# Kernel tuning notes

Hardware: AMD Instinct MI355X
Metric: run time of the kernel (lower is better)

The kernel has to match this reference:

```python
import jax, jax.numpy as jnp
import numpy as np

V, H, O = 50257, 1024, 1024
B, T = 64, 256

def setup_inputs() -> dict:
    key = jax.random.key(0)
    ks = jax.random.split(key, 8)
    s = 1.0 / np.sqrt(H)
    return {
        "input": jax.random.randint(ks[0], (B, T), 0, V),
        "hidden": jnp.zeros((B, H), jnp.float32),
        "emb": jax.random.normal(ks[1], (V, H), jnp.float32),
        "Wi": jax.random.uniform(ks[2], (H, H), jnp.float32, -s, s),
        "bi": jax.random.uniform(ks[3], (H,), jnp.float32, -s, s),
        "Wh": jax.random.uniform(ks[4], (H, H), jnp.float32, -s, s),
        "bh": jax.random.uniform(ks[5], (H,), jnp.float32, -s, s),
        "Wo": jax.random.uniform(ks[6], (H, O), jnp.float32, -s, s),
        "bo": jax.random.uniform(ks[7], (O,), jnp.float32, -s, s),
    }

def reference(input, hidden, emb, Wi, bi, Wh, bh, Wo, bo):
    # embedded: [B, T, H]; precompute the input-to-hidden projection for all steps
    embedded = emb[input]
    ix = jnp.einsum('bth,hk->tbk', embedded, Wi) + bi  # [T, B, H]

    def step(h, ix_t):
        h = jnp.tanh(ix_t + h @ Wh + bh)
        out = h @ Wo + bo
        return h, out

    hidden, outs = jax.lax.scan(step, hidden, ix)  # outs: [T, B, O]
    output_seq = jnp.transpose(outs, (1, 0, 2))    # [B, T, O]
    return output_seq, hidden
```

## Files before the change

### kernel.cpp

```cpp
#include <hip/hip_runtime.h>

typedef unsigned short u16;
typedef unsigned long long u64;
typedef short v8s __attribute__((ext_vector_type(8)));
typedef float v4f __attribute__((ext_vector_type(4)));

__device__ __forceinline__ u16 f2bf(float x) {
    union { float f; unsigned u; } v; v.f = x;
    unsigned r = v.u + 0x7fffu + ((v.u >> 16) & 1u);
    return (u16)(r >> 16);
}

__global__ __launch_bounds__(256) void convert_w(
    const float* __restrict__ Wi, const float* __restrict__ Wh,
    const float* __restrict__ Wo, u16* __restrict__ wi_t,
    u16* __restrict__ wh_t, u16* __restrict__ wo_t) {
    const float* src; u16* dst;
    if (blockIdx.y == 0)      { src = Wi; dst = wi_t; }
    else if (blockIdx.y == 1) { src = Wh; dst = wh_t; }
    else                      { src = Wo; dst = wo_t; }
    int k0 = (blockIdx.x & 31) * 32;
    int n0 = (blockIdx.x >> 5) * 32;
    __shared__ float tile[32][33];
    int t = threadIdx.x;
    {
        int kl = t >> 3, nl4 = (t & 7) * 4;
        float4 v = *(const float4*)(src + (size_t)(k0 + kl) * 1024 + n0 + nl4);
        tile[kl][nl4 + 0] = v.x; tile[kl][nl4 + 1] = v.y;
        tile[kl][nl4 + 2] = v.z; tile[kl][nl4 + 3] = v.w;
    }
    __syncthreads();
    {
        int nl = t >> 3, kl4 = (t & 7) * 4;
        ushort4 o;
        o.x = f2bf(tile[kl4 + 0][nl]); o.y = f2bf(tile[kl4 + 1][nl]);
        o.z = f2bf(tile[kl4 + 2][nl]); o.w = f2bf(tile[kl4 + 3][nl]);
        *(ushort4*)(dst + (size_t)(n0 + nl) * 1024 + k0 + kl4) = o;
    }
}

__global__ __launch_bounds__(256) void gather_emb(
    const int* __restrict__ input, const float* __restrict__ emb,
    u16* __restrict__ Aemb) {
    int r = blockIdx.x * 4 + (threadIdx.x >> 6);
    int lane = threadIdx.x & 63;
    int b = r & 63, t = r >> 6;
    int idx = input[b * 256 + t];
    const float* s = emb + (size_t)idx * 1024;
    u16* d = Aemb + (size_t)r * 1024;
#pragma unroll
    for (int i = 0; i < 4; i++) {
        float4 v = *(const float4*)(s + i * 256 + lane * 4);
        ushort4 o;
        o.x = f2bf(v.x); o.y = f2bf(v.y); o.z = f2bf(v.z); o.w = f2bf(v.w);
        *(ushort4*)(d + i * 256 + lane * 4) = o;
    }
}

__global__ __launch_bounds__(256) void gemm_bias(
    const u16* __restrict__ A, const u16* __restrict__ Bt,
    const float* __restrict__ bias, float* __restrict__ out, int mode) {
    __shared__ u16 lA[128 * 40];
    __shared__ u16 lB[128 * 40];
    const int tid = threadIdx.x;
    const int w = tid >> 6, lane = tid & 63;
    const int l15 = lane & 15, quad = lane >> 4;
    const int m0 = blockIdx.x * 128, n0 = blockIdx.y * 128;
    const int wm = (w & 1) * 64, wn = (w >> 1) * 64;
    const int srow = tid >> 1, shalf = tid & 1;
    const u16* gA = A + (size_t)(m0 + srow) * 1024 + shalf * 16;
    const u16* gB = Bt + (size_t)(n0 + srow) * 1024 + shalf * 16;
    v4f zero = {0.f, 0.f, 0.f, 0.f};
    v4f acc[4][4];
#pragma unroll
    for (int i = 0; i < 4; i++)
#pragma unroll
        for (int j = 0; j < 4; j++) acc[i][j] = zero;

    uint4 ra0 = *(const uint4*)gA;
    uint4 ra1 = *(const uint4*)(gA + 8);
    uint4 rb0 = *(const uint4*)gB;
    uint4 rb1 = *(const uint4*)(gB + 8);

    for (int kt = 0; kt < 32; ++kt) {
        __syncthreads();
        *(uint4*)(lA + srow * 40 + shalf * 16) = ra0;
        *(uint4*)(lA + srow * 40 + shalf * 16 + 8) = ra1;
        *(uint4*)(lB + srow * 40 + shalf * 16) = rb0;
        *(uint4*)(lB + srow * 40 + shalf * 16 + 8) = rb1;
        __syncthreads();
        if (kt < 31) {
            const u16* pA = gA + (kt + 1) * 32;
            const u16* pB = gB + (kt + 1) * 32;
            ra0 = *(const uint4*)pA; ra1 = *(const uint4*)(pA + 8);
            rb0 = *(const uint4*)pB; rb1 = *(const uint4*)(pB + 8);
        }
        v8s af[4], bfv[4];
#pragma unroll
        for (int mt = 0; mt < 4; mt++)
            af[mt] = *(const v8s*)(lA + (wm + mt * 16 + l15) * 40 + quad * 8);
#pragma unroll
        for (int nt = 0; nt < 4; nt++)
            bfv[nt] = *(const v8s*)(lB + (wn + nt * 16 + l15) * 40 + quad * 8);
#pragma unroll
        for (int mt = 0; mt < 4; mt++)
#pragma unroll
            for (int nt = 0; nt < 4; nt++)
                acc[mt][nt] = __builtin_amdgcn_mfma_f32_16x16x32_bf16(
                    af[mt], bfv[nt], acc[mt][nt], 0, 0, 0);
    }
#pragma unroll
    for (int nt = 0; nt < 4; nt++) {
        int coln = n0 + wn + nt * 16 + l15;
        float bv = bias[coln];
#pragma unroll
        for (int mt = 0; mt < 4; mt++) {
            int rbase = m0 + wm + mt * 16 + quad * 4;
#pragma unroll
            for (int r = 0; r < 4; r++) {
                int row = rbase + r;
                int orow = mode ? ((row & 63) * 256 + (row >> 6)) : row;
                out[(size_t)orow * 1024 + coln] = acc[mt][nt][r] + bv;
            }
        }
    }
}

__global__ __launch_bounds__(256, 1) void rnn_step_all(
    const u16* __restrict__ wh_t, const float* __restrict__ bh,
    const float* __restrict__ ix, u64* __restrict__ h_buf64,
    u16* __restrict__ h_all, float* __restrict__ out_tail,
    unsigned* __restrict__ flags) {
    const int tid = threadIdx.x, w = tid >> 6, lane = tid & 63;
    const int g = blockIdx.x, gb = g & 3, gc = g >> 2;
    const int quad = lane >> 4, l15 = lane & 15;
    const int col = gc * 64 + w * 16 + l15;
    __shared__ u16 hts[16 * 1032];

    v8s bfr[32];
#pragma unroll
    for (int kc = 0; kc < 32; kc++)
        bfr[kc] = *(const v8s*)(wh_t + (size_t)col * 1024 + kc * 32 + quad * 8);
    const float bhv = bh[col];
    const int mrow0 = gb * 16 + quad * 4;
    const int srow = tid >> 4, sseg = tid & 15;

    for (int t = 0; t < 256; t++) {
        float ixv[4];
        {
            const float* ixp = ix + ((size_t)t * 64 + mrow0) * 1024 + col;
#pragma unroll
            for (int r = 0; r < 4; r++) ixv[r] = ixp[(size_t)r * 1024];
        }
        v4f acc = {0.f, 0.f, 0.f, 0.f};
        if (t > 0) {
            if (tid == 0) {
                const unsigned* fp = flags + t * 4 + gb;
                int cnt = 0;
                while (__hip_atomic_load(fp, __ATOMIC_RELAXED,
                                         __HIP_MEMORY_SCOPE_AGENT) < 16u) {
                    if (++cnt > (1 << 20)) break;
                }
            }
            __syncthreads();
            const u64* hsrc =
                h_buf64 + (size_t)(t & 1) * 16384 + (gb * 16 + srow) * 256;
            u64 tmp[16];
#pragma unroll
            for (int i = 0; i < 16; i++)
                tmp[i] = __hip_atomic_load(hsrc + sseg + i * 16,
                                           __ATOMIC_RELAXED,
                                           __HIP_MEMORY_SCOPE_AGENT);
#pragma unroll
            for (int i = 0; i < 16; i++)
                *(u64*)(hts + srow * 1032 + (sseg + i * 16) * 4) = tmp[i];
            __syncthreads();
#pragma unroll
            for (int kc = 0; kc < 32; kc++) {
                v8s a = *(const v8s*)(hts + l15 * 1032 + kc * 32 + quad * 8);
                acc = __builtin_amdgcn_mfma_f32_16x16x32_bf16(a, bfr[kc], acc,
                                                              0, 0, 0);
            }
        }
        float hv[4]; u16 hb[4];
#pragma unroll
        for (int r = 0; r < 4; r++) {
            float pre = acc[r] + ixv[r] + bhv;
            hv[r] = tanhf(pre);
            hb[r] = f2bf(hv[r]);
        }
        u64* hdst = h_buf64 + (size_t)((t + 1) & 1) * 16384;
#pragma unroll
        for (int r = 0; r < 4; r++) {
            unsigned own = hb[r];
            unsigned other = __shfl_xor(own, 1);
            unsigned p = own | (other << 16);
            unsigned p2 = __shfl_xor(p, 2);
            if ((lane & 3) == 0) {
                u64 q = (u64)p | ((u64)p2 << 32);
                __hip_atomic_store(hdst + (mrow0 + r) * 256 + (col >> 2), q,
                                   __ATOMIC_RELAXED, __HIP_MEMORY_SCOPE_AGENT);
            }
        }
        __syncthreads();
        if (tid == 0)
            __hip_atomic_fetch_add(flags + (t + 1) * 4 + gb, 1u,
                                   __ATOMIC_RELAXED, __HIP_MEMORY_SCOPE_AGENT);
        u16* hall = h_all + (size_t)t * 65536;
#pragma unroll
        for (int r = 0; r < 4; r++) {
            hall[(size_t)(mrow0 + r) * 1024 + col] = hb[r];
            if (t == 255) out_tail[(mrow0 + r) * 1024 + col] = hv[r];
        }
    }
}

extern "C" void kernel_launch(void* const* d_in, const int* in_sizes, int n_in,
                              void* d_out, int out_size, void* d_ws,
                              size_t ws_size, hipStream_t stream) {
    const int*   input = (const int*)d_in[0];
    const float* emb = (const float*)d_in[2];
    const float* Wi  = (const float*)d_in[3];
    const float* bi  = (const float*)d_in[4];
    const float* Wh  = (const float*)d_in[5];
    const float* bh  = (const float*)d_in[6];
    const float* Wo  = (const float*)d_in[7];
    const float* bo  = (const float*)d_in[8];
    float* out = (float*)d_out;
    char* ws = (char*)d_ws;

    u16* wi_t  = (u16*)(ws);
    u16* wh_t  = (u16*)(ws + (2ull << 20));
    u16* wo_t  = (u16*)(ws + (4ull << 20));
    u16* Aemb  = (u16*)(ws + (6ull << 20));
    u64* h_buf = (u64*)(ws + (38ull << 20));
    unsigned* flags = (unsigned*)(ws + (38ull << 20) + (512ull << 10));

    float* ix = out;
    float* out_tail = out + 16777216ull;

    hipMemsetAsync(flags, 0, 8192, stream);
    convert_w<<<dim3(1024, 3), 256, 0, stream>>>(Wi, Wh, Wo, wi_t, wh_t, wo_t);
    gather_emb<<<4096, 256, 0, stream>>>(input, emb, Aemb);
    gemm_bias<<<dim3(128, 8), 256, 0, stream>>>(Aemb, wi_t, bi, ix, 0);
    rnn_step_all<<<64, 256, 0, stream>>>(wh_t, bh, ix, h_buf, Aemb, out_tail,
                                         flags);
    gemm_bias<<<dim3(128, 8), 256, 0, stream>>>(Aemb, wo_t, bo, out, 1);
}
```

Measured before the change: 1.118 ms.

## Replace flag-counter barrier with sentinel polling on per-step hidden buffer

Drops the atomic flag counters and the per-step block-wide sync before signalling. Each step's hidden state now goes straight into the per-timestep h_all buffer, which is pre-filled with 0xFF. Consumers poll their own 8-byte chunks until no sentinel value is left, which removes a round trip through the flag. It also adds double-buffered, XOR-swizzled LDS for the h tile, splits the MFMA chain across four accumulators, and issues the h loads early. The cost is an extra 32MB memset, and the scheme breaks if a real bf16 pair ever packs to all-ones (a NaN pattern, so unlikely).

```diff
diff --git a/kernel.cpp b/kernel.cpp
--- a/kernel.cpp
+++ b/kernel.cpp
@@ -128,14 +128,13 @@
 
 __global__ __launch_bounds__(256, 1) void rnn_step_all(
     const u16* __restrict__ wh_t, const float* __restrict__ bh,
-    const float* __restrict__ ix, u64* __restrict__ h_buf64,
-    u16* __restrict__ h_all, float* __restrict__ out_tail,
-    unsigned* __restrict__ flags) {
+    const float* __restrict__ ix, u16* __restrict__ h_all,
+    float* __restrict__ out_tail) {
     const int tid = threadIdx.x, w = tid >> 6, lane = tid & 63;
     const int g = blockIdx.x, gb = g & 3, gc = g >> 2;
     const int quad = lane >> 4, l15 = lane & 15;
     const int col = gc * 64 + w * 16 + l15;
-    __shared__ u16 hts[16 * 1032];
+    __shared__ u16 hts[2][16 * 1024];
 
     v8s bfr[32];
 #pragma unroll
@@ -144,52 +143,67 @@
     const float bhv = bh[col];
     const int mrow0 = gb * 16 + quad * 4;
     const int srow = tid >> 4, sseg = tid & 15;
+    u64* const hbase = (u64*)h_all;
 
     for (int t = 0; t < 256; t++) {
+        u64 tmp[16];
+        const u64* hsrc = hbase + (size_t)(t ? t - 1 : 0) * 16384 +
+                          (size_t)(gb * 16 + srow) * 256 + sseg;
+        if (t > 0) {
+#pragma unroll
+            for (int i = 0; i < 16; i++)
+                tmp[i] = __hip_atomic_load(hsrc + i * 16, __ATOMIC_RELAXED,
+                                           __HIP_MEMORY_SCOPE_AGENT);
+        }
         float ixv[4];
         {
             const float* ixp = ix + ((size_t)t * 64 + mrow0) * 1024 + col;
 #pragma unroll
             for (int r = 0; r < 4; r++) ixv[r] = ixp[(size_t)r * 1024];
         }
-        v4f acc = {0.f, 0.f, 0.f, 0.f};
+        char* htile = (char*)hts[t & 1];
         if (t > 0) {
-            if (tid == 0) {
-                const unsigned* fp = flags + t * 4 + gb;
-                int cnt = 0;
-                while (__hip_atomic_load(fp, __ATOMIC_RELAXED,
-                                         __HIP_MEMORY_SCOPE_AGENT) < 16u) {
-                    if (++cnt > (1 << 20)) break;
-                }
-            }
-            __syncthreads();
-            const u64* hsrc =
-                h_buf64 + (size_t)(t & 1) * 16384 + (gb * 16 + srow) * 256;
-            u64 tmp[16];
-#pragma unroll
-            for (int i = 0; i < 16; i++)
-                tmp[i] = __hip_atomic_load(hsrc + sseg + i * 16,
-                                           __ATOMIC_RELAXED,
-                                           __HIP_MEMORY_SCOPE_AGENT);
-#pragma unroll
-            for (int i = 0; i < 16; i++)
-                *(u64*)(hts + srow * 1032 + (sseg + i * 16) * 4) = tmp[i];
-            __syncthreads();
+            int guard = 0; bool again = true;
+            while (again) {
+                again = false;
+#pragma unroll
+                for (int i = 0; i < 16; i++)
+                    if (tmp[i] == 0xFFFFFFFFFFFFFFFFull) {
+                        tmp[i] = __hip_atomic_load(hsrc + i * 16,
+                                                   __ATOMIC_RELAXED,
+                                                   __HIP_MEMORY_SCOPE_AGENT);
+                        again = true;
+                    }
+                if (++guard > (1 << 20)) break;
+            }
+#pragma unroll
+            for (int i = 0; i < 16; i++) {
+                int wbyte = ((sseg + i * 16) * 8) ^ ((srow & 7) << 4);
+                *(u64*)(htile + srow * 2048 + wbyte) = tmp[i];
+            }
+        }
+        __syncthreads();
+        v4f acc[4];
+#pragma unroll
+        for (int j = 0; j < 4; j++) acc[j] = (v4f){0.f, 0.f, 0.f, 0.f};
+        if (t > 0) {
 #pragma unroll
             for (int kc = 0; kc < 32; kc++) {
-                v8s a = *(const v8s*)(hts + l15 * 1032 + kc * 32 + quad * 8);
-                acc = __builtin_amdgcn_mfma_f32_16x16x32_bf16(a, bfr[kc], acc,
-                                                              0, 0, 0);
+                int rbyte = (kc * 64 + quad * 16) ^ ((l15 & 7) << 4);
+                v8s a = *(const v8s*)(htile + l15 * 2048 + rbyte);
+                acc[kc & 3] = __builtin_amdgcn_mfma_f32_16x16x32_bf16(
+                    a, bfr[kc], acc[kc & 3], 0, 0, 0);
             }
         }
         float hv[4]; u16 hb[4];
 #pragma unroll
         for (int r = 0; r < 4; r++) {
-            float pre = acc[r] + ixv[r] + bhv;
+            float pre = acc[0][r] + acc[1][r] + acc[2][r] + acc[3][r] +
+                        ixv[r] + bhv;
             hv[r] = tanhf(pre);
             hb[r] = f2bf(hv[r]);
         }
-        u64* hdst = h_buf64 + (size_t)((t + 1) & 1) * 16384;
+        u64* hdst = hbase + (size_t)t * 16384;
 #pragma unroll
         for (int r = 0; r < 4; r++) {
             unsigned own = hb[r];
@@ -202,15 +216,10 @@
                                    __ATOMIC_RELAXED, __HIP_MEMORY_SCOPE_AGENT);
             }
         }
-        __syncthreads();
-        if (tid == 0)
-            __hip_atomic_fetch_add(flags + (t + 1) * 4 + gb, 1u,
-                                   __ATOMIC_RELAXED, __HIP_MEMORY_SCOPE_AGENT);
-        u16* hall = h_all + (size_t)t * 65536;
-#pragma unroll
-        for (int r = 0; r < 4; r++) {
-            hall[(size_t)(mrow0 + r) * 1024 + col] = hb[r];
-            if (t == 255) out_tail[(mrow0 + r) * 1024 + col] = hv[r];
+        if (t == 255) {
+#pragma unroll
+            for (int r = 0; r < 4; r++)
+                out_tail[(mrow0 + r) * 1024 + col] = hv[r];
         }
     }
 }
@@ -233,17 +242,14 @@
     u16* wh_t  = (u16*)(ws + (2ull << 20));
     u16* wo_t  = (u16*)(ws + (4ull << 20));
     u16* Aemb  = (u16*)(ws + (6ull << 20));
-    u64* h_buf = (u64*)(ws + (38ull << 20));
-    unsigned* flags = (unsigned*)(ws + (38ull << 20) + (512ull << 10));
 
     float* ix = out;
     float* out_tail = out + 16777216ull;
 
-    hipMemsetAsync(flags, 0, 8192, stream);
     convert_w<<<dim3(1024, 3), 256, 0, stream>>>(Wi, Wh, Wo, wi_t, wh_t, wo_t);
     gather_emb<<<4096, 256, 0, stream>>>(input, emb, Aemb);
     gemm_bias<<<dim3(128, 8), 256, 0, stream>>>(Aemb, wi_t, bi, ix, 0);
-    rnn_step_all<<<64, 256, 0, stream>>>(wh_t, bh, ix, h_buf, Aemb, out_tail,
-                                         flags);
+    hipMemsetAsync(Aemb, 0xFF, 33554432ull, stream);
+    rnn_step_all<<<64, 256, 0, stream>>>(wh_t, bh, ix, Aemb, out_tail);
     gemm_bias<<<dim3(128, 8), 256, 0, stream>>>(Aemb, wo_t, bo, out, 1);
 }
```

After: 1.253 ms. +12.0%, slower.

## Per-wave flag signaling, double-buffered swizzled LDS h tile, split MFMA accumulators

Applied to the files above, without the earlier changes.

Each wave now waits on and increments the step flag itself, with the target count raised to 64, instead of one thread per block. This drops one __syncthreads per step and uses s_waitcnt to order the h stores before the flag update. The LDS h tile is double-buffered and XOR-swizzled instead of padded, so only one block barrier per step remains. The MFMA chain is split across four accumulators to break the dependency chain, and h_all stores are packed into 64-bit writes. The intent is to shorten the serial per-step latency of the recurrence, at the cost of more flag atomics and more delicate memory-ordering correctness.

```diff
diff --git a/kernel.cpp b/kernel.cpp
--- a/kernel.cpp
+++ b/kernel.cpp
@@ -135,7 +135,7 @@
     const int g = blockIdx.x, gb = g & 3, gc = g >> 2;
     const int quad = lane >> 4, l15 = lane & 15;
     const int col = gc * 64 + w * 16 + l15;
-    __shared__ u16 hts[16 * 1032];
+    __shared__ u16 hts[2][16 * 1024];
 
     v8s bfr[32];
 #pragma unroll
@@ -152,17 +152,17 @@
 #pragma unroll
             for (int r = 0; r < 4; r++) ixv[r] = ixp[(size_t)r * 1024];
         }
-        v4f acc = {0.f, 0.f, 0.f, 0.f};
+        char* htile = (char*)hts[t & 1];
         if (t > 0) {
-            if (tid == 0) {
+            if ((tid & 63) == 0) {
                 const unsigned* fp = flags + t * 4 + gb;
                 int cnt = 0;
                 while (__hip_atomic_load(fp, __ATOMIC_RELAXED,
-                                         __HIP_MEMORY_SCOPE_AGENT) < 16u) {
+                                         __HIP_MEMORY_SCOPE_AGENT) < 64u) {
                     if (++cnt > (1 << 20)) break;
                 }
             }
-            __syncthreads();
+            asm volatile("" ::: "memory");
             const u64* hsrc =
                 h_buf64 + (size_t)(t & 1) * 16384 + (gb * 16 + srow) * 256;
             u64 tmp[16];
@@ -172,44 +172,54 @@
                                            __ATOMIC_RELAXED,
                                            __HIP_MEMORY_SCOPE_AGENT);
 #pragma unroll
-            for (int i = 0; i < 16; i++)
-                *(u64*)(hts + srow * 1032 + (sseg + i * 16) * 4) = tmp[i];
-            __syncthreads();
+            for (int i = 0; i < 16; i++) {
+                int wbyte = ((sseg + i * 16) * 8) ^ ((srow & 7) << 4);
+                *(u64*)(htile + srow * 2048 + wbyte) = tmp[i];
+            }
+        }
+        __syncthreads();
+        v4f acc[4];
+#pragma unroll
+        for (int j = 0; j < 4; j++) acc[j] = (v4f){0.f, 0.f, 0.f, 0.f};
+        if (t > 0) {
 #pragma unroll
             for (int kc = 0; kc < 32; kc++) {
-                v8s a = *(const v8s*)(hts + l15 * 1032 + kc * 32 + quad * 8);
-                acc = __builtin_amdgcn_mfma_f32_16x16x32_bf16(a, bfr[kc], acc,
-                                                              0, 0, 0);
+                int rbyte = (kc * 64 + quad * 16) ^ ((l15 & 7) << 4);
+                v8s a = *(const v8s*)(htile + l15 * 2048 + rbyte);
+                acc[kc & 3] = __builtin_amdgcn_mfma_f32_16x16x32_bf16(
+                    a, bfr[kc], acc[kc & 3], 0, 0, 0);
             }
         }
         float hv[4]; u16 hb[4];
 #pragma unroll
         for (int r = 0; r < 4; r++) {
-            float pre = acc[r] + ixv[r] + bhv;
+            float pre = acc[0][r] + acc[1][r] + acc[2][r] + acc[3][r] +
+                        ixv[r] + bhv;
             hv[r] = tanhf(pre);
             hb[r] = f2bf(hv[r]);
         }
         u64* hdst = h_buf64 + (size_t)((t + 1) & 1) * 16384;
+        u64 qs[4];
 #pragma unroll
         for (int r = 0; r < 4; r++) {
             unsigned own = hb[r];
             unsigned other = __shfl_xor(own, 1);
             unsigned p = own | (other << 16);
             unsigned p2 = __shfl_xor(p, 2);
-            if ((lane & 3) == 0) {
-                u64 q = (u64)p | ((u64)p2 << 32);
-                __hip_atomic_store(hdst + (mrow0 + r) * 256 + (col >> 2), q,
+            qs[r] = (u64)p | ((u64)p2 << 32);
+            if ((lane & 3) == 0)
+                __hip_atomic_store(hdst + (mrow0 + r) * 256 + (col >> 2), qs[r],
                                    __ATOMIC_RELAXED, __HIP_MEMORY_SCOPE_AGENT);
-            }
-        }
-        __syncthreads();
-        if (tid == 0)
+        }
+        asm volatile("s_waitcnt vmcnt(0)" ::: "memory");
+        if ((tid & 63) == 0)
             __hip_atomic_fetch_add(flags + (t + 1) * 4 + gb, 1u,
                                    __ATOMIC_RELAXED, __HIP_MEMORY_SCOPE_AGENT);
-        u16* hall = h_all + (size_t)t * 65536;
+        u64* hall64 = (u64*)(h_all + (size_t)t * 65536);
 #pragma unroll
         for (int r = 0; r < 4; r++) {
-            hall[(size_t)(mrow0 + r) * 1024 + col] = hb[r];
+            if ((lane & 3) == 0)
+                hall64[(mrow0 + r) * 256 + (col >> 2)] = qs[r];
             if (t == 255) out_tail[(mrow0 + r) * 1024 + col] = hv[r];
         }
     }
```

Result: slower. 1.518 ms (+35.8%).

## Use direct global-to-LDS loads in GEMM and fast tanh in recurrence

Applied to the files above, without the earlier changes.

The input-projection GEMM now stages A and B tiles with global_load_lds (direct global-to-LDS DMA) instead of loading into registers and then storing to shared memory. This drops the register round trip and the LDS row padding, but also removes the register prefetch of the next k-tile and may add bank conflicts on the unpadded layout. In the serial recurrence, tanhf is replaced by an exp2/rcp based approximation to shorten the per-step critical path, at a small accuracy cost.

```diff
diff --git a/kernel.cpp b/kernel.cpp
--- a/kernel.cpp
+++ b/kernel.cpp
@@ -9,6 +9,11 @@
     union { float f; unsigned u; } v; v.f = x;
     unsigned r = v.u + 0x7fffu + ((v.u >> 16) & 1u);
     return (u16)(r >> 16);
+}
+
+__device__ __forceinline__ float tanh_fast(float x) {
+    float e = __builtin_amdgcn_exp2f(x * 2.88539008177793f);
+    return __builtin_fmaf(-2.0f, __builtin_amdgcn_rcpf(e + 1.0f), 1.0f);
 }
 
 __global__ __launch_bounds__(256) void convert_w(
@@ -60,16 +65,18 @@
 __global__ __launch_bounds__(256) void gemm_bias(
     const u16* __restrict__ A, const u16* __restrict__ Bt,
     const float* __restrict__ bias, float* __restrict__ out, int mode) {
-    __shared__ u16 lA[128 * 40];
-    __shared__ u16 lB[128 * 40];
+    __shared__ u16 lA[128 * 32];
+    __shared__ u16 lB[128 * 32];
     const int tid = threadIdx.x;
     const int w = tid >> 6, lane = tid & 63;
     const int l15 = lane & 15, quad = lane >> 4;
     const int m0 = blockIdx.x * 128, n0 = blockIdx.y * 128;
     const int wm = (w & 1) * 64, wn = (w >> 1) * 64;
-    const int srow = tid >> 1, shalf = tid & 1;
-    const u16* gA = A + (size_t)(m0 + srow) * 1024 + shalf * 16;
-    const u16* gB = Bt + (size_t)(n0 + srow) * 1024 + shalf * 16;
+    const u16* gA = A + (size_t)m0 * 1024;
+    const u16* gB = Bt + (size_t)n0 * 1024;
+    auto* ldsA = (__attribute__((address_space(3))) u16*)lA;
+    auto* ldsB = (__attribute__((address_space(3))) u16*)lB;
+
     v4f zero = {0.f, 0.f, 0.f, 0.f};
     v4f acc[4][4];
 #pragma unroll
@@ -77,31 +84,30 @@
 #pragma unroll
         for (int j = 0; j < 4; j++) acc[i][j] = zero;
 
-    uint4 ra0 = *(const uint4*)gA;
-    uint4 ra1 = *(const uint4*)(gA + 8);
-    uint4 rb0 = *(const uint4*)gB;
-    uint4 rb1 = *(const uint4*)(gB + 8);
-
     for (int kt = 0; kt < 32; ++kt) {
         __syncthreads();
-        *(uint4*)(lA + srow * 40 + shalf * 16) = ra0;
-        *(uint4*)(lA + srow * 40 + shalf * 16 + 8) = ra1;
-        *(uint4*)(lB + srow * 40 + shalf * 16) = rb0;
-        *(uint4*)(lB + srow * 40 + shalf * 16 + 8) = rb1;
+#pragma unroll
+        for (int j = 0; j < 2; j++) {
+            int idx = (w * 2 + j) * 64 + lane;
+            int row = idx >> 2, ch = idx & 3;
+            size_t goff = (size_t)row * 1024 + kt * 32 + ch * 8;
+            __builtin_amdgcn_global_load_lds(
+                (const __attribute__((address_space(1))) unsigned*)(gA + goff),
+                (__attribute__((address_space(3))) unsigned*)(ldsA + idx * 8),
+                16, 0, 0);
+            __builtin_amdgcn_global_load_lds(
+                (const __attribute__((address_space(1))) unsigned*)(gB + goff),
+                (__attribute__((address_space(3))) unsigned*)(ldsB + idx * 8),
+                16, 0, 0);
+        }
         __syncthreads();
-        if (kt < 31) {
-            const u16* pA = gA + (kt + 1) * 32;
-            const u16* pB = gB + (kt + 1) * 32;
-            ra0 = *(const uint4*)pA; ra1 = *(const uint4*)(pA + 8);
-            rb0 = *(const uint4*)pB; rb1 = *(const uint4*)(pB + 8);
-        }
         v8s af[4], bfv[4];
 #pragma unroll
         for (int mt = 0; mt < 4; mt++)
-            af[mt] = *(const v8s*)(lA + (wm + mt * 16 + l15) * 40 + quad * 8);
+            af[mt] = *(const v8s*)(lA + (wm + mt * 16 + l15) * 32 + quad * 8);
 #pragma unroll
         for (int nt = 0; nt < 4; nt++)
-            bfv[nt] = *(const v8s*)(lB + (wn + nt * 16 + l15) * 40 + quad * 8);
+            bfv[nt] = *(const v8s*)(lB + (wn + nt * 16 + l15) * 32 + quad * 8);
 #pragma unroll
         for (int mt = 0; mt < 4; mt++)
 #pragma unroll
@@ -186,7 +192,7 @@
 #pragma unroll
         for (int r = 0; r < 4; r++) {
             float pre = acc[r] + ixv[r] + bhv;
-            hv[r] = tanhf(pre);
+            hv[r] = tanh_fast(pre);
             hb[r] = f2bf(hv[r]);
         }
         u64* hdst = h_buf64 + (size_t)((t + 1) & 1) * 16384;
```

New measurement: 1.149 ms. 2.8% more time.
